# Optimization experiments

Hardware: AMD Instinct MI355X
Metric: run time of the kernel (lower is better)

## Reference

```python
import jax, jax.numpy as jnp
import numpy as np

N, IN_DIM, OUT_DIM = 8192, 1024, 1024

def setup_inputs() -> dict:
    key = jax.random.key(0)
    k1, k2, k3, k4 = jax.random.split(key, 4)
    return {
        "input_feature": jax.random.normal(k1, (N, IN_DIM), dtype=jnp.float32),
        "wq": jax.random.normal(k2, (IN_DIM, OUT_DIM), dtype=jnp.float32),
        "wk": jax.random.normal(k3, (IN_DIM, OUT_DIM), dtype=jnp.float32),
        "wv": jax.random.normal(k4, (IN_DIM, OUT_DIM), dtype=jnp.float32),
    }

def reference(input_feature, wq, wk, wv):
    # QKV projections: [N, out_dim]
    q = input_feature @ wq
    k = input_feature @ wk
    v = input_feature @ wv
    # Attention scores [N, N]; note: original applies NO 1/sqrt(d) scaling
    scores = q @ k.T
    attn = jax.nn.softmax(scores, axis=1)
    return attn @ v
```

## Files before the change

kernel.cpp:

```cpp
#include <hip/hip_runtime.h>
#include <hip/hip_bf16.h>
#include <math.h>

#define NROWS 8192
#define DIM   1024
#define CAP   256
#define MARGIN 120.0f

using f16x8 = __attribute__((ext_vector_type(8))) _Float16;
using f32x4 = __attribute__((ext_vector_type(4))) float;
typedef unsigned short u16;
typedef unsigned int   u32;

#define AS1 __attribute__((address_space(1)))
#define AS3 __attribute__((address_space(3)))

__global__ __launch_bounds__(256) void split2h(const float* __restrict__ X,
                                               u16* __restrict__ H,
                                               u16* __restrict__ L) {
    const int idx = (blockIdx.x * 256 + threadIdx.x) * 4;
    float4 x = *(const float4*)&X[idx];
    float c[4] = {x.x, x.y, x.z, x.w};
    u16 h[4], l[4];
#pragma unroll
    for (int i = 0; i < 4; ++i) {
        _Float16 hh = (_Float16)c[i];
        float r = c[i] - (float)hh;
        _Float16 ll = (_Float16)r;
        h[i] = *(u16*)&hh; l[i] = *(u16*)&ll;
    }
    *(ushort4*)&H[idx] = make_ushort4(h[0], h[1], h[2], h[3]);
    *(ushort4*)&L[idx] = make_ushort4(l[0], l[1], l[2], l[3]);
}

__global__ __launch_bounds__(256) void split_wvt(const float* __restrict__ W,
                                                 u16* __restrict__ H) {
    __shared__ float t[64][65];
    const int k0 = blockIdx.x * 64, n0 = blockIdx.y * 64;
    const int c = threadIdx.x & 63, r4 = threadIdx.x >> 6;
#pragma unroll
    for (int i = 0; i < 16; ++i) {
        int k = r4 + i * 4;
        t[k][c] = W[(size_t)(k0 + k) * DIM + n0 + c];
    }
    __syncthreads();
#pragma unroll
    for (int i = 0; i < 16; ++i) {
        int n = r4 + i * 4;
        _Float16 hb = (_Float16)t[c][n];
        H[(n0 + n) * DIM + k0 + c] = *(u16*)&hb;
    }
}

template<int NP>
__device__ __forceinline__ void gemm_lds(const u16* const (&Ap)[NP],
                                         const u16* const (&Bp)[NP],
                                         int row0, int col0, f32x4 (&acc)[4][4],
                                         short (&As)[2][4096], short (&Bs)[2][4096]) {
    const int tid = threadIdx.x;
    const int w = tid >> 6, lane = tid & 63;
    const int wy = w >> 1, wx = w & 1;
    const int quad = lane >> 4, r16 = lane & 15;

    const int    srow   = w * 32 + (lane >> 2);
    const int    schunk = ((lane & 3) ^ ((lane >> 3) & 3)) * 8;
    const size_t gA0 = (size_t)(row0 + srow) * DIM + schunk;
    const size_t gA1 = gA0 + (size_t)16 * DIM;
    const size_t gB0 = (size_t)(col0 + srow) * DIM + schunk;
    const size_t gB1 = gB0 + (size_t)16 * DIM;
    const int lds0 = (w * 32) * 32;
    const int lds1 = (w * 32 + 16) * 32;

    auto issue = [&](const u16* A, const u16* B, size_t ko, int buf) {
        __builtin_amdgcn_global_load_lds((const AS1 u32*)(A + gA0 + ko), (AS3 u32*)&As[buf][lds0], 16, 0, 0);
        __builtin_amdgcn_global_load_lds((const AS1 u32*)(A + gA1 + ko), (AS3 u32*)&As[buf][lds1], 16, 0, 0);
        __builtin_amdgcn_global_load_lds((const AS1 u32*)(B + gB0 + ko), (AS3 u32*)&Bs[buf][lds0], 16, 0, 0);
        __builtin_amdgcn_global_load_lds((const AS1 u32*)(B + gB1 + ko), (AS3 u32*)&Bs[buf][lds1], 16, 0, 0);
    };

    issue(Ap[0], Bp[0], 0, 0);

    const int ccol = (quad ^ ((r16 >> 1) & 3)) * 8;

    int pp = 0;
#pragma unroll
    for (int p = 0; p < NP; ++p) {
        const u16* A = Ap[p];
        const u16* B = Bp[p];
        const u16* An = (p + 1 < NP) ? Ap[p + 1] : A;
        const u16* Bn = (p + 1 < NP) ? Bp[p + 1] : B;
        const bool more = (p + 1 < NP);
        for (int i = 0; i < 32; ++i) {
            __syncthreads();
            const int cur = pp, nxt = pp ^ 1;
            if (i < 31)      issue(A, B, (size_t)(i + 1) * 32, nxt);
            else if (more)   issue(An, Bn, 0, nxt);
            const short* AsC = As[cur];
            const short* BsC = Bs[cur];
            f16x8 af[4], bfr[4];
#pragma unroll
            for (int m = 0; m < 4; ++m)
                af[m] = *(const f16x8*)&AsC[(wy * 64 + m * 16 + r16) * 32 + ccol];
#pragma unroll
            for (int n = 0; n < 4; ++n)
                bfr[n] = *(const f16x8*)&BsC[(wx * 64 + n * 16 + r16) * 32 + ccol];
#pragma unroll
            for (int m = 0; m < 4; ++m)
#pragma unroll
                for (int n = 0; n < 4; ++n)
                    acc[m][n] = __builtin_amdgcn_mfma_f32_16x16x32_f16(af[m], bfr[n], acc[m][n], 0, 0, 0);
            pp ^= 1;
        }
    }
}

__global__ __launch_bounds__(256) void g_gemm(const u16* __restrict__ Wkh, const u16* __restrict__ Wkl,
                                              const u16* __restrict__ Wqh, const u16* __restrict__ Wql,
                                              float* __restrict__ Gt) {
    __shared__ short As[2][4096], Bs[2][4096];
    const int tid = threadIdx.x, w = tid >> 6, lane = tid & 63;
    const int wy = w >> 1, wx = w & 1, quad = lane >> 4, r16 = lane & 15;
    const int row0 = blockIdx.y * 128, col0 = blockIdx.x * 128;
    const u16* const Ap[3] = { Wkl, Wkh, Wkh };
    const u16* const Bp[3] = { Wqh, Wql, Wqh };
    f32x4 acc[4][4] = {};
    gemm_lds<3>(Ap, Bp, row0, col0, acc, As, Bs);
#pragma unroll
    for (int m = 0; m < 4; ++m)
#pragma unroll
        for (int n = 0; n < 4; ++n)
#pragma unroll
            for (int reg = 0; reg < 4; ++reg) {
                const int row = row0 + wy * 64 + m * 16 + quad * 4 + reg;
                const int col = col0 + wx * 64 + n * 16 + r16;
                Gt[row * DIM + col] = acc[m][n][reg];
            }
}

__global__ __launch_bounds__(256) void yv_gemm(const u16* __restrict__ Xh, const u16* __restrict__ Xl,
                                               const u16* __restrict__ Gth, const u16* __restrict__ Gtl,
                                               const u16* __restrict__ Wvth,
                                               float* __restrict__ Y, u16* __restrict__ Yh, u16* __restrict__ Vh) {
    __shared__ short As[2][4096], Bs[2][4096];
    const int tid = threadIdx.x, w = tid >> 6, lane = tid & 63;
    const int wy = w >> 1, wx = w & 1, quad = lane >> 4, r16 = lane & 15;
    const int id = blockIdx.x;
    const int z = id >> 9;
    const int within = id & 511;
    const int colt = within >> 6;
    const int rowt = within & 63;
    const int row0 = rowt * 128, col0 = colt * 128;
    f32x4 acc[4][4] = {};
    if (z == 0) {
        const u16* const Ap[3] = { Xl,  Xh,  Xh  };
        const u16* const Bp[3] = { Gth, Gtl, Gth };
        gemm_lds<3>(Ap, Bp, row0, col0, acc, As, Bs);
#pragma unroll
        for (int m = 0; m < 4; ++m)
#pragma unroll
            for (int n = 0; n < 4; ++n)
#pragma unroll
                for (int reg = 0; reg < 4; ++reg) {
                    const int row = row0 + wy * 64 + m * 16 + quad * 4 + reg;
                    const int col = col0 + wx * 64 + n * 16 + r16;
                    float v = acc[m][n][reg];
                    Y[row * DIM + col] = v;
                    _Float16 hb = (_Float16)v;
                    Yh[row * DIM + col] = *(u16*)&hb;
                }
    } else {
        const u16* const Ap[1] = { Xh };
        const u16* const Bp[1] = { Wvth };
        gemm_lds<1>(Ap, Bp, row0, col0, acc, As, Bs);
#pragma unroll
        for (int m = 0; m < 4; ++m)
#pragma unroll
            for (int n = 0; n < 4; ++n)
#pragma unroll
                for (int reg = 0; reg < 4; ++reg) {
                    const int row = row0 + wy * 64 + m * 16 + quad * 4 + reg;
                    const int col = col0 + wx * 64 + n * 16 + r16;
                    _Float16 hb = (_Float16)acc[m][n][reg];
                    Vh[row * DIM + col] = *(u16*)&hb;
                }
    }
}

__global__ __launch_bounds__(256) void filter_kernel(const u16* __restrict__ Yhp,
                                                     const u16* __restrict__ Xhp,
                                                     int* __restrict__ cnt,
                                                     int2* __restrict__ cand) {
    __shared__ short As[2][4096], Bs[2][4096];
    const int tid = threadIdx.x, w = tid >> 6, lane = tid & 63;
    const int wy = w >> 1, wx = w & 1, quad = lane >> 4, r16 = lane & 15;
    const int id = blockIdx.x;
    const int colt = id >> 6;
    const int rowt = id & 63;
    const int row0 = rowt * 128, col0 = colt * 128;

    const u16* const Ap[1] = { Yhp };
    const u16* const Bp[1] = { Xhp };
    f32x4 acc[4][4] = {};
    gemm_lds<1>(Ap, Bp, row0, col0, acc, As, Bs);

#pragma unroll
    for (int m = 0; m < 4; ++m) {
#pragma unroll
        for (int reg = 0; reg < 4; ++reg) {
            float mx = fmaxf(fmaxf(acc[m][0][reg], acc[m][1][reg]),
                             fmaxf(acc[m][2][reg], acc[m][3][reg]));
            mx = fmaxf(mx, __shfl_xor(mx, 1, 64));
            mx = fmaxf(mx, __shfl_xor(mx, 2, 64));
            mx = fmaxf(mx, __shfl_xor(mx, 4, 64));
            mx = fmaxf(mx, __shfl_xor(mx, 8, 64));
            const float th = mx - MARGIN;
            const int row = row0 + wy * 64 + m * 16 + quad * 4 + reg;
#pragma unroll
            for (int n = 0; n < 4; ++n) {
                float s = acc[m][n][reg];
                if (s >= th) {
                    int pos = atomicAdd(&cnt[row], 1);
                    if (pos < CAP)
                        cand[(size_t)row * CAP + pos] =
                            make_int2(col0 + wx * 64 + n * 16 + r16, __float_as_int(s));
                }
            }
        }
    }
}

__global__ __launch_bounds__(256) void finalize_kernel(const float* __restrict__ Y,
                                                       const float* __restrict__ X,
                                                       const u16* __restrict__ Vh,
                                                       const int* __restrict__ cnt,
                                                       const int2* __restrict__ cand,
                                                       float* __restrict__ out) {
    const int i = blockIdx.x;
    const int tid = threadIdx.x;
    const int w = tid >> 6, lane = tid & 63;
    __shared__ float  red[256];
    __shared__ int    surv[64];
    __shared__ double sprec[64];
    __shared__ float  wgt[64];
    __shared__ int    nsurv;

    const int c = min(cnt[i], CAP);
    float m = -3.0e38f;
    for (int t = tid; t < c; t += 256)
        m = fmaxf(m, __int_as_float(cand[(size_t)i * CAP + t].y));
    red[tid] = m;
    __syncthreads();
    for (int s = 128; s > 0; s >>= 1) {
        if (tid < s) red[tid] = fmaxf(red[tid], red[tid + s]);
        __syncthreads();
    }
    const float th = red[0] - MARGIN;
    if (tid == 0) nsurv = 0;
    __syncthreads();
    for (int t = tid; t < c; t += 256) {
        int2 e = cand[(size_t)i * CAP + t];
        if (__int_as_float(e.y) >= th) {
            int p = atomicAdd(&nsurv, 1);
            if (p < 64) surv[p] = e.x;
        }
    }
    __syncthreads();
    const int ns = min(nsurv, 64);
    for (int u = w; u < ns; u += 4) {
        const int j = surv[u];
        double a = 0.0;
        for (int d = lane; d < DIM; d += 64)
            a += (double)Y[(size_t)i * DIM + d] * (double)X[(size_t)j * DIM + d];
#pragma unroll
        for (int o = 32; o > 0; o >>= 1)
            a += __shfl_down(a, o, 64);
        if (lane == 0) sprec[u] = a;
    }
    __syncthreads();
    if (tid == 0) {
        double mm = -1.0e300;
        for (int u = 0; u < ns; ++u) mm = fmax(mm, sprec[u]);
        double l = 0.0;
        for (int u = 0; u < ns; ++u) l += exp(sprec[u] - mm);
        for (int u = 0; u < ns; ++u) wgt[u] = (float)(exp(sprec[u] - mm) / l);
    }
    __syncthreads();
    for (int d = tid; d < DIM; d += 256) {
        float o = 0.f;
        for (int u = 0; u < ns; ++u) {
            _Float16 hv = *(const _Float16*)&Vh[(size_t)surv[u] * DIM + d];
            o += wgt[u] * (float)hv;
        }
        out[(size_t)i * DIM + d] = o;
    }
}

extern "C" void kernel_launch(void* const* d_in, const int* in_sizes, int n_in,
                              void* d_out, int out_size, void* d_ws, size_t ws_size,
                              hipStream_t stream) {
    const float* X  = (const float*)d_in[0];
    const float* wq = (const float*)d_in[1];
    const float* wk = (const float*)d_in[2];
    const float* wv = (const float*)d_in[3];
    float* out = (float*)d_out;

    char* ws = (char*)d_ws;
    const size_t MB = 1024 * 1024;
    u16*   Xh   = (u16*)(ws +   0 * MB);
    u16*   Xl   = (u16*)(ws +  16 * MB);
    u16*   Wqh  = (u16*)(ws +  32 * MB);
    u16*   Wql  = (u16*)(ws +  34 * MB);
    u16*   Wkh  = (u16*)(ws +  36 * MB);
    u16*   Wkl  = (u16*)(ws +  38 * MB);
    u16*   Wvth = (u16*)(ws +  40 * MB);
    float* Gt   = (float*)(ws + 42 * MB);
    u16*   Gth  = (u16*)(ws +  46 * MB);
    u16*   Gtl  = (u16*)(ws +  48 * MB);
    float* Y    = (float*)(ws + 64 * MB);
    u16*   Yh   = (u16*)(ws +  96 * MB);
    u16*   Vh   = (u16*)(ws + 112 * MB);
    int*   cnt  = (int*)(ws + 128 * MB);
    int2*  cand = (int2*)(ws + 129 * MB);

    hipMemsetAsync(cnt, 0, (size_t)NROWS * 4, stream);

    split2h<<<NROWS * DIM / 1024, 256, 0, stream>>>(X, Xh, Xl);
    split2h<<<DIM * DIM / 1024, 256, 0, stream>>>(wq, Wqh, Wql);
    split2h<<<DIM * DIM / 1024, 256, 0, stream>>>(wk, Wkh, Wkl);
    split_wvt<<<dim3(16, 16), 256, 0, stream>>>(wv, Wvth);

    g_gemm<<<dim3(8, 8), 256, 0, stream>>>(Wkh, Wkl, Wqh, Wql, Gt);
    split2h<<<DIM * DIM / 1024, 256, 0, stream>>>(Gt, Gth, Gtl);

    yv_gemm<<<1024, 256, 0, stream>>>(Xh, Xl, Gth, Gtl, Wvth, Y, Yh, Vh);

    filter_kernel<<<4096, 256, 0, stream>>>(Yh, Xh, cnt, cand);

    finalize_kernel<<<NROWS, 256, 0, stream>>>(Y, X, Vh, cnt, cand, out);
}
```

Measured before the change: 533.4 us.

## Add triple-buffered async-LDS GEMM pipeline and vectorize refine-kernel loads

Introduces gemm_pipe, a three-stage LDS ring buffer that uses global_load_lds with vmcnt-based waits, a single barrier per k-step and inline ds_read_b128 with sched barriers around the MFMA block. yv_gemm and filter_kernel switch to it with launch bounds of 3 blocks per CU. The refine kernel's dot products use float4 loads and its output accumulation reads fp16 pairs. The goal is to hide global-load latency and cut barrier overhead in the dominant GEMMs. In exchange LDS use grows by half, which may limit occupancy, and the hand-written waitcnt logic is fragile.

```diff
diff --git a/kernel.cpp b/kernel.cpp
--- a/kernel.cpp
+++ b/kernel.cpp
@@ -14,6 +14,9 @@
 
 #define AS1 __attribute__((address_space(1)))
 #define AS3 __attribute__((address_space(3)))
+
+#define DS_READ_B128(dst, off) \
+    asm volatile("ds_read_b128 %0, %1" : "=v"(dst) : "v"(off))
 
 __global__ __launch_bounds__(256) void split2h(const float* __restrict__ X,
                                                u16* __restrict__ H,
@@ -114,6 +117,83 @@
     }
 }
 
+template<int NP>
+__device__ __forceinline__ void gemm_pipe(const u16* const (&Ap)[NP],
+                                          const u16* const (&Bp)[NP],
+                                          int row0, int col0, f32x4 (&acc)[4][4],
+                                          short (&As)[3][4096], short (&Bs)[3][4096]) {
+    const int tid = threadIdx.x;
+    const int w = tid >> 6, lane = tid & 63;
+    const int wy = w >> 1, wx = w & 1;
+    const int quad = lane >> 4, r16 = lane & 15;
+
+    const int    srow   = w * 32 + (lane >> 2);
+    const int    schunk = ((lane & 3) ^ ((lane >> 3) & 3)) * 8;
+    const size_t gA0 = (size_t)(row0 + srow) * DIM + schunk;
+    const size_t gA1 = gA0 + (size_t)16 * DIM;
+    const size_t gB0 = (size_t)(col0 + srow) * DIM + schunk;
+    const size_t gB1 = gB0 + (size_t)16 * DIM;
+    const int lds0 = (w * 32) * 32;
+    const int lds1 = (w * 32 + 16) * 32;
+
+    auto stage = [&](int g, int b) {
+        const u16* A; const u16* B;
+        if (NP == 1) { A = Ap[0]; B = Bp[0]; }
+        else {
+            const int p = g >> 5;
+            A = (p == 0) ? Ap[0] : (p == 1) ? Ap[1] : Ap[NP - 1];
+            B = (p == 0) ? Bp[0] : (p == 1) ? Bp[1] : Bp[NP - 1];
+        }
+        const size_t ko = (size_t)(g & 31) * 32;
+        __builtin_amdgcn_global_load_lds((const AS1 u32*)(A + gA0 + ko), (AS3 u32*)&As[b][lds0], 16, 0, 0);
+        __builtin_amdgcn_global_load_lds((const AS1 u32*)(A + gA1 + ko), (AS3 u32*)&As[b][lds1], 16, 0, 0);
+        __builtin_amdgcn_global_load_lds((const AS1 u32*)(B + gB0 + ko), (AS3 u32*)&Bs[b][lds0], 16, 0, 0);
+        __builtin_amdgcn_global_load_lds((const AS1 u32*)(B + gB1 + ko), (AS3 u32*)&Bs[b][lds1], 16, 0, 0);
+    };
+
+    const int ccol = (quad ^ ((r16 >> 1) & 3)) * 8;
+    u32 aA[4], aB[4];
+#pragma unroll
+    for (int m = 0; m < 4; ++m)
+        aA[m] = (u32)(uintptr_t)&As[0][(wy * 64 + m * 16 + r16) * 32 + ccol];
+#pragma unroll
+    for (int n = 0; n < 4; ++n)
+        aB[n] = (u32)(uintptr_t)&Bs[0][(wx * 64 + n * 16 + r16) * 32 + ccol];
+
+    auto body = [&](u32 bo) {
+        f16x8 af[4], bfr[4];
+#pragma unroll
+        for (int m = 0; m < 4; ++m) DS_READ_B128(af[m], aA[m] + bo);
+#pragma unroll
+        for (int n = 0; n < 4; ++n) DS_READ_B128(bfr[n], aB[n] + bo);
+        asm volatile("s_waitcnt lgkmcnt(0)");
+        __builtin_amdgcn_sched_barrier(0);
+#pragma unroll
+        for (int m = 0; m < 4; ++m)
+#pragma unroll
+            for (int n = 0; n < 4; ++n)
+                acc[m][n] = __builtin_amdgcn_mfma_f32_16x16x32_f16(af[m], bfr[n], acc[m][n], 0, 0, 0);
+        __builtin_amdgcn_sched_barrier(0);
+    };
+
+    const int NK = NP * 32;
+    stage(0, 0);
+    stage(1, 1);
+
+    int buf = 0;
+#pragma unroll 1
+    for (int g = 0; g < NK - 1; ++g) {
+        asm volatile("s_waitcnt vmcnt(4)");
+        __builtin_amdgcn_s_barrier();
+        if (g + 2 < NK) stage(g + 2, (buf == 0) ? 2 : buf - 1);
+        body((u32)buf * 8192u);
+        buf = (buf == 2) ? 0 : buf + 1;
+    }
+    asm volatile("s_waitcnt vmcnt(0)");
+    __builtin_amdgcn_s_barrier();
+    body((u32)buf * 8192u);
+}
+
 __global__ __launch_bounds__(256) void g_gemm(const u16* __restrict__ Wkh, const u16* __restrict__ Wkl,
                                               const u16* __restrict__ Wqh, const u16* __restrict__ Wql,
                                               float* __restrict__ Gt) {
@@ -137,11 +217,11 @@
             }
 }
 
-__global__ __launch_bounds__(256) void yv_gemm(const u16* __restrict__ Xh, const u16* __restrict__ Xl,
-                                               const u16* __restrict__ Gth, const u16* __restrict__ Gtl,
-                                               const u16* __restrict__ Wvth,
-                                               float* __restrict__ Y, u16* __restrict__ Yh, u16* __restrict__ Vh) {
-    __shared__ short As[2][4096], Bs[2][4096];
+__global__ __launch_bounds__(256, 3) void yv_gemm(const u16* __restrict__ Xh, const u16* __restrict__ Xl,
+                                                  const u16* __restrict__ Gth, const u16* __restrict__ Gtl,
+                                                  const u16* __restrict__ Wvth,
+                                                  float* __restrict__ Y, u16* __restrict__ Yh, u16* __restrict__ Vh) {
+    __shared__ short As[3][4096], Bs[3][4096];
     const int tid = threadIdx.x, w = tid >> 6, lane = tid & 63;
     const int wy = w >> 1, wx = w & 1, quad = lane >> 4, r16 = lane & 15;
     const int id = blockIdx.x;
@@ -154,7 +234,7 @@
     if (z == 0) {
         const u16* const Ap[3] = { Xl,  Xh,  Xh  };
         const u16* const Bp[3] = { Gth, Gtl, Gth };
-        gemm_lds<3>(Ap, Bp, row0, col0, acc, As, Bs);
+        gemm_pipe<3>(Ap, Bp, row0, col0, acc, As, Bs);
 #pragma unroll
         for (int m = 0; m < 4; ++m)
 #pragma unroll
@@ -171,7 +251,7 @@
     } else {
         const u16* const Ap[1] = { Xh };
         const u16* const Bp[1] = { Wvth };
-        gemm_lds<1>(Ap, Bp, row0, col0, acc, As, Bs);
+        gemm_pipe<1>(Ap, Bp, row0, col0, acc, As, Bs);
 #pragma unroll
         for (int m = 0; m < 4; ++m)
 #pragma unroll
@@ -186,11 +266,11 @@
     }
 }
 
-__global__ __launch_bounds__(256) void filter_kernel(const u16* __restrict__ Yhp,
-                                                     const u16* __restrict__ Xhp,
-                                                     int* __restrict__ cnt,
-                                                     int2* __restrict__ cand) {
-    __shared__ short As[2][4096], Bs[2][4096];
+__global__ __launch_bounds__(256, 3) void filter_kernel(const u16* __restrict__ Yhp,
+                                                        const u16* __restrict__ Xhp,
+                                                        int* __restrict__ cnt,
+                                                        int2* __restrict__ cand) {
+    __shared__ short As[3][4096], Bs[3][4096];
     const int tid = threadIdx.x, w = tid >> 6, lane = tid & 63;
     const int wy = w >> 1, wx = w & 1, quad = lane >> 4, r16 = lane & 15;
     const int id = blockIdx.x;
@@ -201,7 +281,7 @@
     const u16* const Ap[1] = { Yhp };
     const u16* const Bp[1] = { Xhp };
     f32x4 acc[4][4] = {};
-    gemm_lds<1>(Ap, Bp, row0, col0, acc, As, Bs);
+    gemm_pipe<1>(Ap, Bp, row0, col0, acc, As, Bs);
 
 #pragma unroll
     for (int m = 0; m < 4; ++m) {
@@ -269,8 +349,13 @@
     for (int u = w; u < ns; u += 4) {
         const int j = surv[u];
         double a = 0.0;
-        for (int d = lane; d < DIM; d += 64)
-            a += (double)Y[(size_t)i * DIM + d] * (double)X[(size_t)j * DIM + d];
+#pragma unroll 1
+        for (int d4 = lane; d4 < DIM / 4; d4 += 64) {
+            float4 yv = *(const float4*)&Y[(size_t)i * DIM + d4 * 4];
+            float4 xv = *(const float4*)&X[(size_t)j * DIM + d4 * 4];
+            a += (double)yv.x * (double)xv.x + (double)yv.y * (double)xv.y
+               + (double)yv.z * (double)xv.z + (double)yv.w * (double)xv.w;
+        }
 #pragma unroll
         for (int o = 32; o > 0; o >>= 1)
             a += __shfl_down(a, o, 64);
@@ -285,13 +370,19 @@
         for (int u = 0; u < ns; ++u) wgt[u] = (float)(exp(sprec[u] - mm) / l);
     }
     __syncthreads();
-    for (int d = tid; d < DIM; d += 256) {
-        float o = 0.f;
+    for (int d2 = tid; d2 < DIM / 2; d2 += 256) {
+        float o0 = 0.f, o1 = 0.f;
         for (int u = 0; u < ns; ++u) {
-            _Float16 hv = *(const _Float16*)&Vh[(size_t)surv[u] * DIM + d];
-            o += wgt[u] * (float)hv;
-        }
-        out[(size_t)i * DIM + d] = o;
+            const u16* vp = &Vh[(size_t)surv[u] * DIM + d2 * 2];
+            u32 pair = *(const u32*)vp;
+            _Float16 h0 = *(_Float16*)&pair;
+            u16 hi = (u16)(pair >> 16);
+            _Float16 h1 = *(_Float16*)&hi;
+            o0 += wgt[u] * (float)h0;
+            o1 += wgt[u] * (float)h1;
+        }
+        out[(size_t)i * DIM + d2 * 2]     = o0;
+        out[(size_t)i * DIM + d2 * 2 + 1] = o1;
     }
 }
 
```

Result: no change. 527.5 us (-1.1%).
